# Kernel optimization log

Hardware: AMD Instinct MI355X
Metric: run time of the kernel (lower is better)

Reference implementation:

```python
import jax, jax.numpy as jnp
from jax import lax
import numpy as np

V, E, H, B, T = 512, 512, 1024, 128, 512

def _xavier(key, shape):
    fan_out, fan_in = shape
    bound = float(np.sqrt(6.0 / (fan_in + fan_out)))
    return jax.random.uniform(key, shape, jnp.float32, -bound, bound)

def setup_inputs() -> dict:
    key = jax.random.key(0)
    ks = jax.random.split(key, 6)
    src = jax.random.randint(ks[0], (B, T), 0, V, dtype=jnp.int32)
    embedding = _xavier(ks[1], (V, E))
    w_ih_l0 = _xavier(ks[2], (3 * H, E))
    w_hh_l0 = _xavier(ks[3], (3 * H, H))
    w_ih_l1 = _xavier(ks[4], (3 * H, H))
    w_hh_l1 = _xavier(ks[5], (3 * H, H))
    zb = jnp.zeros((3 * H,), jnp.float32)  # biases init'd to 0 in module
    return {
        "src": src, "embedding": embedding,
        "w_ih_l0": w_ih_l0, "w_hh_l0": w_hh_l0, "b_ih_l0": zb, "b_hh_l0": zb,
        "w_ih_l1": w_ih_l1, "w_hh_l1": w_hh_l1, "b_ih_l1": zb, "b_hh_l1": zb,
    }

def _gru_layer(x_seq, w_ih, w_hh, b_ih, b_hh):
    # x_seq: [B, T, D]. Precompute all input projections as one big GEMM.
    gates_x = jnp.einsum('btd,gd->btg', x_seq, w_ih) + b_ih  # [B, T, 3H]
    h_dim = w_hh.shape[1]
    w_hh_t = w_hh.T  # [H, 3H]

    def step(h, gx):
        gh = h @ w_hh_t + b_hh                      # [B, 3H]
        xr, xz, xn = jnp.split(gx, 3, axis=-1)
        hr, hz, hn = jnp.split(gh, 3, axis=-1)
        r = jax.nn.sigmoid(xr + hr)
        z = jax.nn.sigmoid(xz + hz)
        n = jnp.tanh(xn + r * hn)
        h_new = (1.0 - z) * n + z * h
        return h_new, h_new

    h0 = jnp.zeros((x_seq.shape[0], h_dim), x_seq.dtype)
    h_last, outs = lax.scan(step, h0, jnp.swapaxes(gates_x, 0, 1))  # time-major scan
    return jnp.swapaxes(outs, 0, 1), h_last  # [B, T, H], [B, H]

def reference(src, embedding, w_ih_l0, w_hh_l0, b_ih_l0, b_hh_l0,
              w_ih_l1, w_hh_l1, b_ih_l1, b_hh_l1):
    x = embedding[src]  # [B, T, E]
    y0, h0 = _gru_layer(x, w_ih_l0, w_hh_l0, b_ih_l0, b_hh_l0)
    _, h1 = _gru_layer(y0, w_ih_l1, w_hh_l1, b_ih_l1, b_hh_l1)
    return jnp.stack([h0, h1], axis=0)  # (n_layers, B, H)
```

## Files before the change

### kernel.cpp

```cpp
#include <hip/hip_runtime.h>

typedef __attribute__((ext_vector_type(8))) short short8;
typedef __attribute__((ext_vector_type(4))) float f32x4;

constexpr int Bsz = 128;
constexpr int Tlen = 512;
constexpr int Hd = 1024;
constexpr int RS = 128 * 1024;

__device__ __forceinline__ unsigned short f2b(float f) {
  unsigned int u = __float_as_uint(f);
  u = (u + 0x7FFFu + ((u >> 16) & 1u)) >> 16;
  return (unsigned short)u;
}
__device__ __forceinline__ unsigned int aload32(const unsigned int* p) {
  return __hip_atomic_load(p, __ATOMIC_RELAXED, __HIP_MEMORY_SCOPE_AGENT);
}
__device__ __forceinline__ void astore32(unsigned int* p, unsigned int v) {
  __hip_atomic_store(p, v, __ATOMIC_RELAXED, __HIP_MEMORY_SCOPE_AGENT);
}

template <int LAYER>
__device__ __forceinline__ void run_layer(
    const int* __restrict__ src, const float* __restrict__ P,
    const unsigned short* __restrict__ Wh, const unsigned short* __restrict__ Wx,
    const float* __restrict__ bhh, const float* __restrict__ bih,
    float* __restrict__ dout,
    unsigned short* __restrict__ A0r,
    unsigned short* __restrict__ A1hr,
    unsigned short* __restrict__ A1xr,
    unsigned int* __restrict__ flags,
    unsigned int* __restrict__ invflags,
    f32x4 (*__restrict__ red)[4][3][64],
    const int R0, const int J0, const int w, const int lane,
    const int tid, const int c, const int xcd, const bool isInv)
{
  constexpr int NQ = LAYER ? 4 : 3;
  const int lrow = lane >> 4;
  const int lcol = lane & 15;
  const int col = J0 + lcol;
  const int mh = R0 >> 6;
  const int dom = LAYER * 2 + mh;

  const float bhr = bhh[col], bhz = bhh[1024 + col], bhn = bhh[2048 + col];
  float gbr = 0.f, gbz = 0.f, gbn = 0.f;
  if (LAYER) { gbr = bih[col]; gbz = bih[1024 + col]; gbn = bih[2048 + col]; }

  short8 wBh[3][8];
#pragma unroll
  for (int g = 0; g < 3; ++g) {
    const unsigned short* wp = Wh + (g * 1024 + col) * 1024 + w * 256 + lrow * 8;
#pragma unroll
    for (int ks = 0; ks < 8; ++ks) wBh[g][ks] = *(const short8*)(wp + ks * 32);
  }
  short8 wBx[3][8];
  if (LAYER) {
#pragma unroll
    for (int g = 0; g < 3; ++g) {
      const unsigned short* wp = Wx + (g * 1024 + col) * 1024 + w * 256 + lrow * 8;
#pragma unroll
      for (int ks = 0; ks < 8; ++ks) wBx[g][ks] = *(const short8*)(wp + ks * 32);
    }
  }

  const int myrow0 = R0 + w * 16 + lrow * 4;
  float hold[4] = {0.f, 0.f, 0.f, 0.f};

  for (int r = 0; r <= 512; ++r) {
    if (LAYER == 0 && r == 512) break;
    const bool active = LAYER ? (r >= 1) : true;

    if (active) {
      const int scur = r & 3, snext = (r + 1) & 3;

      float gpr[4], gpz[4], gpn[4];
      if (LAYER == 0) {
        int sv[4];
#pragma unroll
        for (int i = 0; i < 4; ++i) sv[i] = src[(myrow0 + i) * Tlen + r];
#pragma unroll
        for (int i = 0; i < 4; ++i) {
          const float* pr = P + sv[i] * 3072 + col;
          gpr[i] = pr[0]; gpz[i] = pr[1024]; gpn[i] = pr[2048];
        }
      } else {
#pragma unroll
        for (int i = 0; i < 4; ++i) { gpr[i] = gbr; gpz[i] = gbz; gpn[i] = gbn; }
      }

      const bool doDetect = (LAYER == 1) || (r >= 1);
      if (doDetect) {
        if (w == 0) {
          const unsigned tgt = (unsigned)r;
          if (isInv) {
            const unsigned tA = (r >= 2) ? (unsigned)(r - 2) : 0u;
            const unsigned int* f0 = flags + 0 * 64 + lane;
            const unsigned int* f1 = flags + 1 * 64 + lane;
            const unsigned int* f2 = flags + 2 * 64 + lane;
            const unsigned int* f3 = flags + 3 * 64 + lane;
            for (;;) {
              const unsigned a = aload32(f0), b = aload32(f1),
                             d = aload32(f2), e = aload32(f3);
              if (__all(a >= tgt && b >= tA && d >= tA && e >= tA)) break;
              __builtin_amdgcn_s_sleep(1);
            }
            __builtin_amdgcn_fence(__ATOMIC_ACQUIRE, "agent");
            if (lane == 0) astore32(&invflags[xcd * 16], (unsigned)(r + 1));
          } else {
            const unsigned int* fp = flags + mh * 64 + lane;
            const unsigned int* fs = flags + (2 + mh) * 64 + lane;
            const unsigned tgtS = LAYER ? tgt : ((r >= 2) ? (unsigned)(r - 2) : 0u);
            const unsigned int* iv = &invflags[xcd * 16];
            for (;;) {
              const unsigned a = aload32(fp), b = aload32(fs), k = aload32(iv);
              if (__all(a >= tgt && b >= tgtS && k >= tgt)) break;
              __builtin_amdgcn_s_sleep(1);
            }
          }
        }
        __syncthreads();
        asm volatile("buffer_inv sc0" ::: "memory");
      } else if (isInv) {
        if (w == 0 && lane == 0) astore32(&invflags[xcd * 16], 1u);
      }

      f32x4 ar[4], az[4], anh[4], anx[4];
#pragma unroll
      for (int f = 0; f < 4; ++f) {
        ar[f]  = (f32x4){0.f, 0.f, 0.f, 0.f};
        az[f]  = (f32x4){0.f, 0.f, 0.f, 0.f};
        anh[f] = (f32x4){0.f, 0.f, 0.f, 0.f};
        anx[f] = (f32x4){0.f, 0.f, 0.f, 0.f};
      }

      if (LAYER == 0) {
        if (r >= 1) {
          const unsigned short* rb[4];
#pragma unroll
          for (int f = 0; f < 4; ++f)
            rb[f] = A0r + scur * RS + (R0 + f * 16 + lcol) * 1024 + w * 256 + lrow * 8;
          short8 ab[4][4];
#pragma unroll
          for (int s = 0; s < 4; ++s)
#pragma unroll
            for (int f = 0; f < 4; ++f) ab[s][f] = *(const short8*)(rb[f] + s * 32);
#pragma unroll
          for (int ks = 0; ks < 8; ++ks) {
#pragma unroll
            for (int f = 0; f < 4; ++f) {
              const short8 a = ab[ks & 3][f];
              ar[f]  = __builtin_amdgcn_mfma_f32_16x16x32_bf16(a, wBh[0][ks], ar[f], 0, 0, 0);
              az[f]  = __builtin_amdgcn_mfma_f32_16x16x32_bf16(a, wBh[1][ks], az[f], 0, 0, 0);
              anh[f] = __builtin_amdgcn_mfma_f32_16x16x32_bf16(a, wBh[2][ks], anh[f], 0, 0, 0);
            }
            if (ks + 4 < 8)
#pragma unroll
              for (int f = 0; f < 4; ++f)
                ab[ks & 3][f] = *(const short8*)(rb[f] + (ks + 4) * 32);
          }
        }
      } else {
        const unsigned short* rbx[4];
        const unsigned short* rbh[4];
#pragma unroll
        for (int f = 0; f < 4; ++f) {
          const int ro = (R0 + f * 16 + lcol) * 1024 + w * 256 + lrow * 8;
          rbx[f] = A1xr + scur * RS + ro;
          rbh[f] = A1hr + scur * RS + ro;
        }
        if (r >= 2) {
          short8 ab[4][4];
#pragma unroll
          for (int s = 0; s < 4; ++s)
#pragma unroll
            for (int f = 0; f < 4; ++f) ab[s][f] = *(const short8*)(rbx[f] + s * 32);
#pragma unroll
          for (int ks = 0; ks < 16; ++ks) {
            const short8 br = (ks < 8) ? wBx[0][ks] : wBh[0][ks - 8];
            const short8 bz = (ks < 8) ? wBx[1][ks] : wBh[1][ks - 8];
            const short8 bn = (ks < 8) ? wBx[2][ks] : wBh[2][ks - 8];
#pragma unroll
            for (int f = 0; f < 4; ++f) {
              const short8 a = ab[ks & 3][f];
              ar[f] = __builtin_amdgcn_mfma_f32_16x16x32_bf16(a, br, ar[f], 0, 0, 0);
              az[f] = __builtin_amdgcn_mfma_f32_16x16x32_bf16(a, bz, az[f], 0, 0, 0);
              if (ks < 8)
                anx[f] = __builtin_amdgcn_mfma_f32_16x16x32_bf16(a, bn, anx[f], 0, 0, 0);
              else
                anh[f] = __builtin_amdgcn_mfma_f32_16x16x32_bf16(a, bn, anh[f], 0, 0, 0);
            }
            const int kn = ks + 4;
            if (kn < 16) {
#pragma unroll
              for (int f = 0; f < 4; ++f)
                ab[ks & 3][f] = *(const short8*)(
                    (kn < 8) ? (rbx[f] + kn * 32) : (rbh[f] + (kn - 8) * 32));
            }
          }
        } else {
          short8 ab[4][4];
#pragma unroll
          for (int s = 0; s < 4; ++s)
#pragma unroll
            for (int f = 0; f < 4; ++f) ab[s][f] = *(const short8*)(rbx[f] + s * 32);
#pragma unroll
          for (int ks = 0; ks < 8; ++ks) {
#pragma unroll
            for (int f = 0; f < 4; ++f) {
              const short8 a = ab[ks & 3][f];
              ar[f]  = __builtin_amdgcn_mfma_f32_16x16x32_bf16(a, wBx[0][ks], ar[f], 0, 0, 0);
              az[f]  = __builtin_amdgcn_mfma_f32_16x16x32_bf16(a, wBx[1][ks], az[f], 0, 0, 0);
              anx[f] = __builtin_amdgcn_mfma_f32_16x16x32_bf16(a, wBx[2][ks], anx[f], 0, 0, 0);
            }
            if (ks + 4 < 8)
#pragma unroll
              for (int f = 0; f < 4; ++f)
                ab[ks & 3][f] = *(const short8*)(rbx[f] + (ks + 4) * 32);
          }
        }
      }

#pragma unroll
      for (int f = 0; f < 4; ++f) {
        if (f != w) {
          const int sl = (f < w) ? f : f - 1;
          red[w][0][sl][lane] = ar[f];
          red[w][1][sl][lane] = az[f];
          red[w][2][sl][lane] = anh[f];
          if (NQ == 4) red[w][3][sl][lane] = anx[f];
        }
      }
      __syncthreads();
      f32x4 sr  = (f32x4){0.f, 0.f, 0.f, 0.f};
      f32x4 sz_ = (f32x4){0.f, 0.f, 0.f, 0.f};
      f32x4 snh = (f32x4){0.f, 0.f, 0.f, 0.f};
      f32x4 snx = (f32x4){0.f, 0.f, 0.f, 0.f};
#pragma unroll
      for (int f = 0; f < 4; ++f)
        if (f == w) { sr = ar[f]; sz_ = az[f]; snh = anh[f]; if (NQ == 4) snx = anx[f]; }
#pragma unroll
      for (int ww = 0; ww < 4; ++ww) {
        if (ww != w) {
          const int sl = (w < ww) ? w : w - 1;
          sr  += red[ww][0][sl][lane];
          sz_ += red[ww][1][sl][lane];
          snh += red[ww][2][sl][lane];
          if (NQ == 4) snx += red[ww][3][sl][lane];
        }
      }

      const bool lastw = LAYER ? (r == 512) : (r == 511);
#pragma unroll
      for (int i = 0; i < 4; ++i) {
        const int row = myrow0 + i;
        float rg = sr[i] + gpr[i] + bhr;
        rg = 1.f / (1.f + __expf(-rg));
        float zg = sz_[i] + gpz[i] + bhz;
        zg = 1.f / (1.f + __expf(-zg));
        const float nx = (snx[i] + gpn[i]) + rg * (snh[i] + bhn);
        const float e2 = __expf(2.f * fabsf(nx));
        const float ng = copysignf(1.f - 2.f / (e2 + 1.f), nx);
        const float hnew = (1.f - zg) * ng + zg * hold[i];
        hold[i] = hnew;
        const unsigned int hb = (unsigned int)f2b(hnew);
        const unsigned int nb = (unsigned int)__shfl_down((int)hb, 1, 64);
        if ((lcol & 1) == 0) {
          const unsigned int pv = hb | (nb << 16);
          if (LAYER == 0) {
            astore32((unsigned int*)(A0r + snext * RS + row * 1024 + J0 + lcol), pv);
            astore32((unsigned int*)(A1xr + snext * RS + row * 1024 + J0 + lcol), pv);
          } else {
            astore32((unsigned int*)(A1hr + snext * RS + row * 1024 + J0 + lcol), pv);
          }
        }
        if (lastw) dout[LAYER * (Bsz * Hd) + row * Hd + col] = hnew;
      }
    }

    __syncthreads();
    if (tid == 0) astore32(&flags[dom * 64 + c], (unsigned)(r + 1));
  }
}

__global__ void __launch_bounds__(256, 1) gru_persist(
    const int* __restrict__ src,
    const float* __restrict__ P,
    const unsigned short* __restrict__ Whh0b,
    const unsigned short* __restrict__ Whh1b,
    const unsigned short* __restrict__ Wih1b,
    const float* __restrict__ bhh0,
    const float* __restrict__ bih1,
    const float* __restrict__ bhh1,
    float* __restrict__ dout,
    unsigned short* __restrict__ A0,
    unsigned short* __restrict__ A1h,
    unsigned short* __restrict__ A1x,
    unsigned int* __restrict__ flags,
    unsigned int* __restrict__ invflags,
    int* __restrict__ taken)
{
  __shared__ f32x4 red[4][4][3][64];
  __shared__ int s_work;

  const int tid = threadIdx.x;

  if (tid == 0) {
    unsigned int xcc;
    asm volatile("s_getreg_b32 %0, hwreg(HW_REG_XCC_ID)" : "=s"(xcc));
    const int pref = ((int)(xcc & 7u)) * 32;
    int got = -1;
    for (int j = 0; j < 256; ++j) {
      const int idx = (pref + j) & 255;
      int expected = 0;
      if (__hip_atomic_compare_exchange_strong(&taken[idx], &expected, 1,
              __ATOMIC_RELAXED, __ATOMIC_RELAXED, __HIP_MEMORY_SCOPE_AGENT)) {
        got = idx; break;
      }
    }
    s_work = got;
  }
  __syncthreads();
  const int work = s_work;
  const int xcd_w = work >> 5;
  const int slot = work & 31;
  const int layer = (slot >> 4) & 1;
  const int m = (slot >> 1) & 7;
  const int c = xcd_w * 8 + m;
  const int mh = slot & 1;
  const int R0 = mh * 64;
  const int J0 = c * 16;
  const bool isInv = (slot == 0);

  const int w = tid >> 6;
  const int lane = tid & 63;

  if (layer == 0)
    run_layer<0>(src, P, Whh0b, Wih1b, bhh0, bih1, dout, A0, A1h, A1x,
                 flags, invflags, red, R0, J0, w, lane, tid, c, xcd_w, isInv);
  else
    run_layer<1>(src, P, Whh1b, Wih1b, bhh1, bih1, dout, A0, A1h, A1x,
                 flags, invflags, red, R0, J0, w, lane, tid, c, xcd_w, false);
}

__global__ void __launch_bounds__(256) cvt_k(const float* __restrict__ s,
                                            unsigned short* __restrict__ d, int n) {
  const int i = (blockIdx.x * 256 + threadIdx.x) * 8;
  if (i >= n) return;
  const float4 a = *(const float4*)(s + i);
  const float4 b = *(const float4*)(s + i + 4);
  short8 o;
  o[0] = (short)f2b(a.x); o[1] = (short)f2b(a.y);
  o[2] = (short)f2b(a.z); o[3] = (short)f2b(a.w);
  o[4] = (short)f2b(b.x); o[5] = (short)f2b(b.y);
  o[6] = (short)f2b(b.z); o[7] = (short)f2b(b.w);
  *(short8*)(d + i) = o;
}

__global__ void __launch_bounds__(256) pemb_k(const float* __restrict__ emb,
                                             const float* __restrict__ wih0,
                                             const float* __restrict__ bih0,
                                             float* __restrict__ P) {
  __shared__ float se[64 * 64];
  const int g = blockIdx.x * 256 + threadIdx.x;
  const int v0 = blockIdx.y * 64;
  float acc[64];
#pragma unroll
  for (int i = 0; i < 64; ++i) acc[i] = 0.f;
  for (int kb = 0; kb < 8; ++kb) {
    __syncthreads();
#pragma unroll
    for (int s = 0; s < 4; ++s) {
      const int idx = threadIdx.x + s * 256;
      const int vv = idx >> 4, k4 = (idx & 15) * 4;
      *(float4*)(se + vv * 64 + k4) =
          *(const float4*)(emb + (v0 + vv) * 512 + kb * 64 + k4);
    }
    __syncthreads();
    float4 wv[16];
#pragma unroll
    for (int j = 0; j < 16; ++j)
      wv[j] = *(const float4*)(wih0 + g * 512 + kb * 64 + j * 4);
    for (int vv = 0; vv < 64; ++vv) {
      const float* er = se + vv * 64;
      float s0 = acc[vv];
#pragma unroll
      for (int j = 0; j < 16; ++j) {
        const float4 e = *(const float4*)(er + j * 4);
        s0 += wv[j].x * e.x + wv[j].y * e.y + wv[j].z * e.z + wv[j].w * e.w;
      }
      acc[vv] = s0;
    }
  }
  const float bb = bih0[g];
  for (int vv = 0; vv < 64; ++vv) P[(v0 + vv) * 3072 + g] = acc[vv] + bb;
}

__global__ void zero_k(unsigned int* flags, int* taken, unsigned int* invflags) {
  const int i = threadIdx.x;
  flags[i] = 0u;
  taken[i] = 0;
  if (i < 128) invflags[i] = 0u;
}

extern "C" void kernel_launch(void* const* d_in, const int* in_sizes, int n_in,
                              void* d_out, int out_size, void* d_ws, size_t ws_size,
                              hipStream_t stream) {
  const int* src = (const int*)d_in[0];
  const float* emb = (const float*)d_in[1];
  const float* wih0 = (const float*)d_in[2];
  const float* whh0 = (const float*)d_in[3];
  const float* bih0 = (const float*)d_in[4];
  const float* bhh0 = (const float*)d_in[5];
  const float* wih1 = (const float*)d_in[6];
  const float* whh1 = (const float*)d_in[7];
  const float* bih1 = (const float*)d_in[8];
  const float* bhh1 = (const float*)d_in[9];
  float* dout = (float*)d_out;

  char* p = (char*)d_ws;
  unsigned short* A0    = (unsigned short*)p;
  unsigned short* A1h   = (unsigned short*)(p + 1048576);
  unsigned short* A1x   = (unsigned short*)(p + 2097152);
  unsigned short* Whh0b = (unsigned short*)(p + 3145728);
  unsigned short* Whh1b = (unsigned short*)(p + 9437184);
  unsigned short* Wih1b = (unsigned short*)(p + 15728640);
  float* P              = (float*)(p + 22020096);
  unsigned int* flags   = (unsigned int*)(p + 28311552);
  unsigned int* invflags= (unsigned int*)(p + 28312576);
  int* taken            = (int*)(p + 28313600);

  constexpr int NW = 3072 * 1024;
  hipLaunchKernelGGL(cvt_k, dim3(NW / (256 * 8)), dim3(256), 0, stream, whh0, Whh0b, NW);
  hipLaunchKernelGGL(cvt_k, dim3(NW / (256 * 8)), dim3(256), 0, stream, whh1, Whh1b, NW);
  hipLaunchKernelGGL(cvt_k, dim3(NW / (256 * 8)), dim3(256), 0, stream, wih1, Wih1b, NW);
  hipLaunchKernelGGL(pemb_k, dim3(12, 8), dim3(256), 0, stream, emb, wih0, bih0, P);
  hipLaunchKernelGGL(zero_k, dim3(1), dim3(256), 0, stream, flags, taken, invflags);

  hipLaunchKernelGGL(gru_persist, dim3(256), dim3(256), 0, stream,
                     src, P, Whh0b, Whh1b, Wih1b, bhh0, bih1, bhh1,
                     dout, A0, A1h, A1x, flags, invflags, taken);
}
```

Before: 8.716 ms.

## Split layer-1 wait into input and recurrent phases; add spinning filler blocks

```diff
diff --git a/kernel.cpp b/kernel.cpp
--- a/kernel.cpp
+++ b/kernel.cpp
@@ -88,42 +88,6 @@
         for (int i = 0; i < 4; ++i) { gpr[i] = gbr; gpz[i] = gbz; gpn[i] = gbn; }
       }
 
-      const bool doDetect = (LAYER == 1) || (r >= 1);
-      if (doDetect) {
-        if (w == 0) {
-          const unsigned tgt = (unsigned)r;
-          if (isInv) {
-            const unsigned tA = (r >= 2) ? (unsigned)(r - 2) : 0u;
-            const unsigned int* f0 = flags + 0 * 64 + lane;
-            const unsigned int* f1 = flags + 1 * 64 + lane;
-            const unsigned int* f2 = flags + 2 * 64 + lane;
-            const unsigned int* f3 = flags + 3 * 64 + lane;
-            for (;;) {
-              const unsigned a = aload32(f0), b = aload32(f1),
-                             d = aload32(f2), e = aload32(f3);
-              if (__all(a >= tgt && b >= tA && d >= tA && e >= tA)) break;
-              __builtin_amdgcn_s_sleep(1);
-            }
-            __builtin_amdgcn_fence(__ATOMIC_ACQUIRE, "agent");
-            if (lane == 0) astore32(&invflags[xcd * 16], (unsigned)(r + 1));
-          } else {
-            const unsigned int* fp = flags + mh * 64 + lane;
-            const unsigned int* fs = flags + (2 + mh) * 64 + lane;
-            const unsigned tgtS = LAYER ? tgt : ((r >= 2) ? (unsigned)(r - 2) : 0u);
-            const unsigned int* iv = &invflags[xcd * 16];
-            for (;;) {
-              const unsigned a = aload32(fp), b = aload32(fs), k = aload32(iv);
-              if (__all(a >= tgt && b >= tgtS && k >= tgt)) break;
-              __builtin_amdgcn_s_sleep(1);
-            }
-          }
-        }
-        __syncthreads();
-        asm volatile("buffer_inv sc0" ::: "memory");
-      } else if (isInv) {
-        if (w == 0 && lane == 0) astore32(&invflags[xcd * 16], 1u);
-      }
-
       f32x4 ar[4], az[4], anh[4], anx[4];
 #pragma unroll
       for (int f = 0; f < 4; ++f) {
@@ -135,6 +99,37 @@
 
       if (LAYER == 0) {
         if (r >= 1) {
+          if (w == 0) {
+            const unsigned tgt = (unsigned)r;
+            if (isInv) {
+              const unsigned tA = (r >= 2) ? (unsigned)(r - 2) : 0u;
+              const unsigned int* f0 = flags + 0 * 64 + lane;
+              const unsigned int* f1 = flags + 1 * 64 + lane;
+              const unsigned int* f2 = flags + 2 * 64 + lane;
+              const unsigned int* f3 = flags + 3 * 64 + lane;
+              for (;;) {
+                const unsigned a = aload32(f0), b = aload32(f1),
+                               d = aload32(f2), e = aload32(f3);
+                if (__all(a >= tgt && b >= tA && d >= tA && e >= tA)) break;
+                __builtin_amdgcn_s_sleep(1);
+              }
+              __builtin_amdgcn_fence(__ATOMIC_ACQUIRE, "agent");
+              if (lane == 0) astore32(&invflags[xcd * 16], (unsigned)(r + 1));
+            } else {
+              const unsigned int* fp = flags + mh * 64 + lane;
+              const unsigned int* fs = flags + (2 + mh) * 64 + lane;
+              const unsigned tgtS = (r >= 2) ? (unsigned)(r - 2) : 0u;
+              const unsigned int* iv = &invflags[xcd * 16];
+              for (;;) {
+                const unsigned a = aload32(fp), b = aload32(fs), k = aload32(iv);
+                if (__all(a >= tgt && b >= tgtS && k >= tgt)) break;
+                __builtin_amdgcn_s_sleep(1);
+              }
+            }
+          }
+          __syncthreads();
+          asm volatile("buffer_inv sc0" ::: "memory");
+
           const unsigned short* rb[4];
 #pragma unroll
           for (int f = 0; f < 4; ++f)
@@ -158,46 +153,27 @@
               for (int f = 0; f < 4; ++f)
                 ab[ks & 3][f] = *(const short8*)(rb[f] + (ks + 4) * 32);
           }
+        } else if (isInv) {
+          if (w == 0 && lane == 0) astore32(&invflags[xcd * 16], 1u);
         }
       } else {
-        const unsigned short* rbx[4];
-        const unsigned short* rbh[4];
-#pragma unroll
-        for (int f = 0; f < 4; ++f) {
-          const int ro = (R0 + f * 16 + lcol) * 1024 + w * 256 + lrow * 8;
-          rbx[f] = A1xr + scur * RS + ro;
-          rbh[f] = A1hr + scur * RS + ro;
-        }
-        if (r >= 2) {
-          short8 ab[4][4];
-#pragma unroll
-          for (int s = 0; s < 4; ++s)
-#pragma unroll
-            for (int f = 0; f < 4; ++f) ab[s][f] = *(const short8*)(rbx[f] + s * 32);
-#pragma unroll
-          for (int ks = 0; ks < 16; ++ks) {
-            const short8 br = (ks < 8) ? wBx[0][ks] : wBh[0][ks - 8];
-            const short8 bz = (ks < 8) ? wBx[1][ks] : wBh[1][ks - 8];
-            const short8 bn = (ks < 8) ? wBx[2][ks] : wBh[2][ks - 8];
-#pragma unroll
-            for (int f = 0; f < 4; ++f) {
-              const short8 a = ab[ks & 3][f];
-              ar[f] = __builtin_amdgcn_mfma_f32_16x16x32_bf16(a, br, ar[f], 0, 0, 0);
-              az[f] = __builtin_amdgcn_mfma_f32_16x16x32_bf16(a, bz, az[f], 0, 0, 0);
-              if (ks < 8)
-                anx[f] = __builtin_amdgcn_mfma_f32_16x16x32_bf16(a, bn, anx[f], 0, 0, 0);
-              else
-                anh[f] = __builtin_amdgcn_mfma_f32_16x16x32_bf16(a, bn, anh[f], 0, 0, 0);
-            }
-            const int kn = ks + 4;
-            if (kn < 16) {
-#pragma unroll
-              for (int f = 0; f < 4; ++f)
-                ab[ks & 3][f] = *(const short8*)(
-                    (kn < 8) ? (rbx[f] + kn * 32) : (rbh[f] + (kn - 8) * 32));
-            }
-          }
-        } else {
+        if (w == 0) {
+          const unsigned tgt = (unsigned)r;
+          const unsigned int* fp = flags + mh * 64 + lane;
+          const unsigned int* iv = &invflags[xcd * 16];
+          for (;;) {
+            const unsigned a = aload32(fp), k = aload32(iv);
+            if (__all(a >= tgt && k >= tgt)) break;
+            __builtin_amdgcn_s_sleep(1);
+          }
+        }
+        __syncthreads();
+        asm volatile("buffer_inv sc0" ::: "memory");
+        {
+          const unsigned short* rbx[4];
+#pragma unroll
+          for (int f = 0; f < 4; ++f)
+            rbx[f] = A1xr + scur * RS + (R0 + f * 16 + lcol) * 1024 + w * 256 + lrow * 8;
           short8 ab[4][4];
 #pragma unroll
           for (int s = 0; s < 4; ++s)
@@ -216,6 +192,42 @@
 #pragma unroll
               for (int f = 0; f < 4; ++f)
                 ab[ks & 3][f] = *(const short8*)(rbx[f] + (ks + 4) * 32);
+          }
+        }
+        if (r >= 2) {
+          if (w == 0) {
+            const unsigned tgt = (unsigned)r;
+            const unsigned int* fs = flags + (2 + mh) * 64 + lane;
+            for (;;) {
+              const unsigned b = aload32(fs);
+              if (__all(b >= tgt)) break;
+              __builtin_amdgcn_s_sleep(1);
+            }
+          }
+          __syncthreads();
+          asm volatile("buffer_inv sc0" ::: "memory");
+          const unsigned short* rbh[4];
+#pragma unroll
+          for (int f = 0; f < 4; ++f)
+            rbh[f] = A1hr + scur * RS + (R0 + f * 16 + lcol) * 1024 + w * 256 + lrow * 8;
+          short8 ab[4][4];
+#pragma unroll
+          for (int s = 0; s < 4; ++s)
+#pragma unroll
+            for (int f = 0; f < 4; ++f) ab[s][f] = *(const short8*)(rbh[f] + s * 32);
+#pragma unroll
+          for (int ks = 0; ks < 8; ++ks) {
+#pragma unroll
+            for (int f = 0; f < 4; ++f) {
+              const short8 a = ab[ks & 3][f];
+              ar[f]  = __builtin_amdgcn_mfma_f32_16x16x32_bf16(a, wBh[0][ks], ar[f], 0, 0, 0);
+              az[f]  = __builtin_amdgcn_mfma_f32_16x16x32_bf16(a, wBh[1][ks], az[f], 0, 0, 0);
+              anh[f] = __builtin_amdgcn_mfma_f32_16x16x32_bf16(a, wBh[2][ks], anh[f], 0, 0, 0);
+            }
+            if (ks + 4 < 8)
+#pragma unroll
+              for (int f = 0; f < 4; ++f)
+                ab[ks & 3][f] = *(const short8*)(rbh[f] + (ks + 4) * 32);
           }
         }
       }
@@ -282,7 +294,7 @@
   }
 }
 
-__global__ void __launch_bounds__(256, 1) gru_persist(
+__global__ void __launch_bounds__(256, 2) gru_persist(
     const int* __restrict__ src,
     const float* __restrict__ P,
     const unsigned short* __restrict__ Whh0b,
@@ -303,24 +315,53 @@
   __shared__ int s_work;
 
   const int tid = threadIdx.x;
+  const int lane = tid & 63;
 
   if (tid == 0) {
     unsigned int xcc;
     asm volatile("s_getreg_b32 %0, hwreg(HW_REG_XCC_ID)" : "=s"(xcc));
     const int pref = ((int)(xcc & 7u)) * 32;
     int got = -1;
-    for (int j = 0; j < 256; ++j) {
+    for (int j = 0; j < 32 && got < 0; ++j) {
+      const int idx = pref + j;
+      int expected = 0;
+      if (__hip_atomic_compare_exchange_strong(&taken[idx], &expected, 1,
+              __ATOMIC_RELAXED, __ATOMIC_RELAXED, __HIP_MEMORY_SCOPE_AGENT))
+        got = idx;
+    }
+    for (int j = 0; j < 256 && got < 0; ++j) {
       const int idx = (pref + j) & 255;
       int expected = 0;
       if (__hip_atomic_compare_exchange_strong(&taken[idx], &expected, 1,
-              __ATOMIC_RELAXED, __ATOMIC_RELAXED, __HIP_MEMORY_SCOPE_AGENT)) {
-        got = idx; break;
-      }
+              __ATOMIC_RELAXED, __ATOMIC_RELAXED, __HIP_MEMORY_SCOPE_AGENT))
+        got = idx;
     }
     s_work = got;
   }
   __syncthreads();
   const int work = s_work;
+
+  if (work < 0) {
+    float h0 = 1.00f, h1 = 1.25f, h2 = 1.50f, h3 = 1.75f;
+    float h4 = 2.00f, h5 = 2.25f, h6 = 2.50f, h7 = 2.75f;
+    const float mm = 1.0000001f, ad = 0.0000003f;
+    for (;;) {
+#pragma unroll
+      for (int i = 0; i < 64; ++i) {
+        h0 = __builtin_fmaf(h0, mm, ad); h1 = __builtin_fmaf(h1, mm, ad);
+        h2 = __builtin_fmaf(h2, mm, ad); h3 = __builtin_fmaf(h3, mm, ad);
+        h4 = __builtin_fmaf(h4, mm, ad); h5 = __builtin_fmaf(h5, mm, ad);
+        h6 = __builtin_fmaf(h6, mm, ad); h7 = __builtin_fmaf(h7, mm, ad);
+      }
+      asm volatile("" :: "v"(h0), "v"(h1), "v"(h2), "v"(h3),
+                         "v"(h4), "v"(h5), "v"(h6), "v"(h7));
+      const unsigned a = aload32(&flags[128 + lane]);
+      const unsigned b = aload32(&flags[192 + lane]);
+      if (__all(a >= 513u && b >= 513u)) break;
+    }
+    return;
+  }
+
   const int xcd_w = work >> 5;
   const int slot = work & 31;
   const int layer = (slot >> 4) & 1;
@@ -332,7 +373,6 @@
   const bool isInv = (slot == 0);
 
   const int w = tid >> 6;
-  const int lane = tid & 63;
 
   if (layer == 0)
     run_layer<0>(src, P, Whh0b, Wih1b, bhh0, bih1, dout, A0, A1h, A1x,
@@ -436,7 +476,7 @@
   hipLaunchKernelGGL(pemb_k, dim3(12, 8), dim3(256), 0, stream, emb, wih0, bih0, P);
   hipLaunchKernelGGL(zero_k, dim3(1), dim3(256), 0, stream, flags, taken, invflags);
 
-  hipLaunchKernelGGL(gru_persist, dim3(256), dim3(256), 0, stream,
+  hipLaunchKernelGGL(gru_persist, dim3(512), dim3(256), 0, stream,
                      src, P, Whh0b, Whh1b, Wih1b, bhh0, bih1, bhh1,
                      dout, A0, A1h, A1x, flags, invflags, taken);
 }
```

Measured after the change: 13.26 ms. 1.52x slower.
